# Kernel optimization log

Measured on AMD Instinct MI355X. Metric: run time of the kernel, lower is better.

Reference implementation:

```python
import jax, jax.numpy as jnp
import numpy as np

B, S, D, H = 4, 2048, 768, 12
DH = D // H  # 64


def setup_inputs() -> dict:
    key = jax.random.key(0)
    ks = jax.random.split(key, 7)
    return {
        "sequences": jax.random.normal(ks[0], (B, S, D), dtype=jnp.float32),
        "wq": jax.random.normal(ks[1], (H, DH, DH), dtype=jnp.float32) / np.sqrt(DH),
        "bq": jax.random.normal(ks[2], (H, DH), dtype=jnp.float32) * 0.02,
        "wk": jax.random.normal(ks[3], (H, DH, DH), dtype=jnp.float32) / np.sqrt(DH),
        "bk": jax.random.normal(ks[4], (H, DH), dtype=jnp.float32) * 0.02,
        "wv": jax.random.normal(ks[5], (H, DH, DH), dtype=jnp.float32) / np.sqrt(DH),
        "bv": jax.random.normal(ks[6], (H, DH), dtype=jnp.float32) * 0.02,
    }


def reference(sequences, wq, bq, wk, bk, wv, bv):
    # split channels into heads: [B, S, H, DH]
    xh = sequences.reshape(B, S, H, DH)
    # per-head linear projections (weight applied as x @ W^T + b, matching nn.Linear)
    q = jnp.einsum("bshd,hed->bshe", xh, wq) + bq  # [B,S,H,DH]
    k = jnp.einsum("bshd,hed->bshe", xh, wk) + bk
    v = jnp.einsum("bshd,hed->bshe", xh, wv) + bv
    scale = 1.0 / np.sqrt(DH).astype(np.float32)
    scores = jnp.einsum("bqhd,bkhd->bhqk", q, k) * scale  # [B,H,S,S]
    attn = jax.nn.softmax(scores, axis=-1)
    out = jnp.einsum("bhqk,bkhd->bqhd", attn, v)  # [B,S,H,DH]
    return out.reshape(B, S, D)
```

## Files before the change

kernel.cpp:

```cpp
#include <hip/hip_runtime.h>

#define NB 4
#define NS 2048
#define ND 768
#define NH 12
#define NDH 64
#define XPITCH 72
#define SSCALE 0.18033688011112043f

typedef __bf16 bf16x8 __attribute__((ext_vector_type(8)));
typedef float  f32x4  __attribute__((ext_vector_type(4)));
typedef unsigned int u32;

#define MFMA16(a, b, c) __builtin_amdgcn_mfma_f32_16x16x32_bf16(a, b, c, 0, 0, 0)

__device__ __forceinline__ u32 packbf(float a, float b) {
    u32 ua = __builtin_bit_cast(u32, a) + 0x8000u;
    u32 ub = __builtin_bit_cast(u32, b) + 0x8000u;
    return __builtin_amdgcn_perm(ub, ua, 0x07060302u);
}

__device__ __forceinline__ bf16x8 cvt8(float4 a, float4 b) {
    union { u32 u[4]; bf16x8 v; } r;
    r.u[0] = packbf(a.x, a.y); r.u[1] = packbf(a.z, a.w);
    r.u[2] = packbf(b.x, b.y); r.u[3] = packbf(b.z, b.w);
    return r.v;
}

__device__ __forceinline__ __bf16 f2bf(float f) {
    u32 u = __builtin_bit_cast(u32, f) + 0x8000u;
    unsigned short s = (unsigned short)(u >> 16);
    return __builtin_bit_cast(__bf16, s);
}

__device__ __forceinline__ void gl16(const __bf16* g, __bf16* l) {
    __builtin_amdgcn_global_load_lds(
        (const __attribute__((address_space(1))) unsigned int*)g,
        (__attribute__((address_space(3))) unsigned int*)l,
        16, 0, 0);
}


__global__ __launch_bounds__(256, 4) void proj_kernel(
    const float* __restrict__ x,
    const float* __restrict__ wq, const float* __restrict__ bq,
    const float* __restrict__ wk, const float* __restrict__ bk,
    const float* __restrict__ wv, const float* __restrict__ bv,
    __bf16* __restrict__ qws, __bf16* __restrict__ kws, __bf16* __restrict__ vtws)
{
    const int st = blockIdx.x, h = blockIdx.y, b = blockIdx.z;
    const int s0 = st * 64;
    const int tid = threadIdx.x;

    __shared__ __align__(16) __bf16 Xs[64 * XPITCH];
    __shared__ __align__(16) __bf16 Tv[64 * XPITCH];

    const int r = tid >> 2, f = tid & 3;
    const int lane = tid & 63, w = tid >> 6, col = lane & 15, quad = lane >> 4;

    const size_t wrow = (size_t)(h * NDH + w * 16 + col) * NDH;
    const float* wq0 = wq + wrow + quad * 8;
    const float* wk0 = wk + wrow + quad * 8;
    const float* wv0 = wv + wrow + quad * 8;
    const bf16x8 wqa0 = cvt8(*(const float4*)(wq0),      *(const float4*)(wq0 + 4));
    const bf16x8 wqa1 = cvt8(*(const float4*)(wq0 + 32), *(const float4*)(wq0 + 36));
    const bf16x8 wka0 = cvt8(*(const float4*)(wk0),      *(const float4*)(wk0 + 4));
    const bf16x8 wka1 = cvt8(*(const float4*)(wk0 + 32), *(const float4*)(wk0 + 36));
    const bf16x8 wva0 = cvt8(*(const float4*)(wv0),      *(const float4*)(wv0 + 4));
    const bf16x8 wva1 = cvt8(*(const float4*)(wv0 + 32), *(const float4*)(wv0 + 36));

    float bqs[4], bks[4], bvs[4];
#pragma unroll
    for (int rr = 0; rr < 4; ++rr) {
        const int e = h * NDH + w * 16 + quad * 4 + rr;
        bqs[rr] = bq[e] * SSCALE;
        bks[rr] = bk[e];
        bvs[rr] = bv[e];
    }

    const size_t bh = (size_t)(b * NH + h);

    {
        const float* xrow = x + (size_t)(b * NS + s0 + r) * ND + h * NDH + f * 16;
        const float4 v0 = *(const float4*)(xrow);
        const float4 v1 = *(const float4*)(xrow + 4);
        const float4 v2 = *(const float4*)(xrow + 8);
        const float4 v3 = *(const float4*)(xrow + 12);
        *(bf16x8*)&Xs[r * XPITCH + f * 16]     = cvt8(v0, v1);
        *(bf16x8*)&Xs[r * XPITCH + f * 16 + 8] = cvt8(v2, v3);
    }
    __syncthreads();

    const int e0 = w * 16 + quad * 4;
    const int jj = e0 >> 5;
    const int qa = (e0 >> 3) & 3;
    const int hf = (e0 >> 2) & 1;
    const int Lf = qa * 16 + col;
    const int kt = st >> 1;

#pragma unroll
    for (int nt = 0; nt < 4; ++nt) {
        const bf16x8 xb0 = *(const bf16x8*)&Xs[(nt * 16 + col) * XPITCH + quad * 8];
        const bf16x8 xb1 = *(const bf16x8*)&Xs[(nt * 16 + col) * XPITCH + 32 + quad * 8];
        f32x4 aq = {0.f, 0.f, 0.f, 0.f};
        f32x4 ak = {0.f, 0.f, 0.f, 0.f};
        f32x4 av = {0.f, 0.f, 0.f, 0.f};
        aq = MFMA16(wqa0, xb0, aq); aq = MFMA16(wqa1, xb1, aq);
        ak = MFMA16(wka0, xb0, ak); ak = MFMA16(wka1, xb1, ak);
        av = MFMA16(wva0, xb0, av); av = MFMA16(wva1, xb1, av);

        union { u32 u[2]; uint2 v; } pq, pk;
        pq.u[0] = packbf(fmaf(aq[0], SSCALE, bqs[0]), fmaf(aq[1], SSCALE, bqs[1]));
        pq.u[1] = packbf(fmaf(aq[2], SSCALE, bqs[2]), fmaf(aq[3], SSCALE, bqs[3]));
        pk.u[0] = packbf(ak[0] + bks[0], ak[1] + bks[1]);
        pk.u[1] = packbf(ak[2] + bks[2], ak[3] + bks[3]);

        const int wa = (st & 1) * 2 + (nt >> 1);
        const int mt = nt & 1;
        const size_t kidx = ((((((size_t)bh * 16 + kt) * 4 + wa) * 2 + mt) * 2 + jj) * 64 + Lf) * 8 + hf * 4;
        const size_t qidx = (((((size_t)bh * 32 + st) * 4 + nt) * 2 + jj) * 64 + Lf) * 8 + hf * 4;
        *(uint2*)(kws + kidx) = pk.v;
        *(uint2*)(qws + qidx) = pq.v;

        const int pos = ((nt >> 1) << 5) + ((col >> 2) << 3) + ((nt & 1) << 2) + (col & 3);
#pragma unroll
        for (int rr = 0; rr < 4; ++rr)
            Tv[(w * 16 + quad * 4 + rr) * XPITCH + pos] = f2bf(av[rr] + bvs[rr]);
    }
    __syncthreads();

    {
        const uint4 v0 = *(const uint4*)&Tv[r * XPITCH + f * 16];
        const uint4 v1 = *(const uint4*)&Tv[r * XPITCH + f * 16 + 8];
        const int wv_ = (st & 1) * 2 + (f >> 1);
        const int dtv = r >> 4;
        const int colv = r & 15;
        const int L0 = ((f & 1) * 2 + 0) * 16 + colv;
        const int L1 = ((f & 1) * 2 + 1) * 16 + colv;
        const size_t vbase = (((size_t)bh * 16 + kt) * 4 + wv_) * 4 + dtv;
        *(uint4*)(vtws + (vbase * 64 + L0) * 8) = v0;
        *(uint4*)(vtws + (vbase * 64 + L1) * 8) = v1;
    }
}

__global__ __launch_bounds__(256, 4) void attn_kernel(
    const __bf16* __restrict__ qws, const __bf16* __restrict__ kws,
    const __bf16* __restrict__ vtws, float* __restrict__ out)
{
    const int bid = blockIdx.x;
    const int xcd = bid & 7;
    const int j   = bid >> 3;
    const int g   = xcd * 6 + (j >> 5);
    const int qt  = j & 31;
    const int h   = g % NH;
    const int b   = g / NH;

    const int q0 = qt * 64;
    const int tid = threadIdx.x;

    __shared__ __align__(16) unsigned char smem[33280];
    __bf16* ldsK = (__bf16*)smem;
    float* slab  = (float*)smem;
    float* lbuf  = (float*)(smem + 32768);

    const size_t bh = (size_t)(b * NH + h);
    const int lane = tid & 63, w = tid >> 6, col = lane & 15, quad = lane >> 4;
    const int wq = w >> 1, wk = w & 1;

    bf16x8 qb0[2], qb1[2];
    {
        const __bf16* qp = qws + (size_t)bh * 131072 + (size_t)qt * 4096
                         + wq * 2048 + lane * 8;
#pragma unroll
        for (int nt = 0; nt < 2; ++nt) {
            qb0[nt] = *(const bf16x8*)(qp + nt * 1024);
            qb1[nt] = *(const bf16x8*)(qp + nt * 1024 + 512);
        }
    }

    const __bf16* kg = kws  + (size_t)bh * 131072 + wk * 2048 + lane * 8;
    const __bf16* vg = vtws + (size_t)bh * 131072 + wk * 2048 + lane * 8;
    __bf16* lk0 = ldsK + w * 2048;
    __bf16* lk1 = ldsK + 8192 + w * 2048;
    const __bf16* lkr0 = lk0 + lane * 8;
    const __bf16* lkr1 = lk1 + lane * 8;

    float l[2] = {0.f, 0.f};
    f32x4 o[4][2];
#pragma unroll
    for (int dt = 0; dt < 4; ++dt)
#pragma unroll
        for (int nt = 0; nt < 2; ++nt) o[dt][nt] = (f32x4){0.f, 0.f, 0.f, 0.f};

#define ATTN_ITER(ktv, LKRD, LKN, DMA_C, PV_LAST) do {                        \
        const __bf16* _vp = vg + (size_t)(ktv) * 4096;                        \
        const bf16x8 va0 = *(const bf16x8*)(_vp);                             \
        const bf16x8 va1 = *(const bf16x8*)(_vp + 512);                       \
        const bf16x8 va2 = *(const bf16x8*)(_vp + 1024);                      \
        const bf16x8 va3 = *(const bf16x8*)(_vp + 1536);                      \
        __builtin_amdgcn_sched_barrier(0);                                    \
        asm volatile("s_waitcnt vmcnt(4)" ::: "memory");                      \
        __builtin_amdgcn_sched_barrier(0);                                    \
        const bf16x8 ka00 = *(const bf16x8*)(LKRD);                           \
        const bf16x8 ka01 = *(const bf16x8*)(LKRD + 512);                     \
        const bf16x8 ka10 = *(const bf16x8*)(LKRD + 1024);                    \
        const bf16x8 ka11 = *(const bf16x8*)(LKRD + 1536);                    \
        if (DMA_C) {                                                          \
            const __bf16* _kn = kg + (size_t)((ktv) + 1) * 4096;              \
            gl16(_kn,        LKN);        gl16(_kn + 512,  LKN + 512);        \
            gl16(_kn + 1024, LKN + 1024); gl16(_kn + 1536, LKN + 1536);       \
        }                                                                     \
        union { u32 u[4]; bf16x8 v; } pb[2];                                  \
        _Pragma("unroll")                                                     \
        for (int nt = 0; nt < 2; ++nt) {                                      \
            f32x4 sA = {0.f, 0.f, 0.f, 0.f};                                  \
            f32x4 sB = {0.f, 0.f, 0.f, 0.f};                                  \
            sA = MFMA16(ka00, qb0[nt], sA); sA = MFMA16(ka01, qb1[nt], sA);   \
            sB = MFMA16(ka10, qb0[nt], sB); sB = MFMA16(ka11, qb1[nt], sB);   \
            const float p0 = __builtin_amdgcn_exp2f(sA[0]);                   \
            const float p1 = __builtin_amdgcn_exp2f(sA[1]);                   \
            const float p2 = __builtin_amdgcn_exp2f(sA[2]);                   \
            const float p3 = __builtin_amdgcn_exp2f(sA[3]);                   \
            const float p4 = __builtin_amdgcn_exp2f(sB[0]);                   \
            const float p5 = __builtin_amdgcn_exp2f(sB[1]);                   \
            const float p6 = __builtin_amdgcn_exp2f(sB[2]);                   \
            const float p7 = __builtin_amdgcn_exp2f(sB[3]);                   \
            l[nt] += ((p0 + p1) + (p2 + p3)) + ((p4 + p5) + (p6 + p7));       \
            pb[nt].u[0] = packbf(p0, p1);                                     \
            pb[nt].u[1] = packbf(p2, p3);                                     \
            pb[nt].u[2] = packbf(p4, p5);                                     \
            pb[nt].u[3] = packbf(p6, p7);                                     \
        }                                                                     \
        __builtin_amdgcn_sched_barrier(0);                                    \
        if (PV_LAST) { asm volatile("s_waitcnt vmcnt(0)" ::: "memory"); }     \
        else         { asm volatile("s_waitcnt vmcnt(4)" ::: "memory"); }     \
        __builtin_amdgcn_sched_barrier(0);                                    \
        _Pragma("unroll")                                                     \
        for (int nt = 0; nt < 2; ++nt) {                                      \
            o[0][nt] = MFMA16(va0, pb[nt].v, o[0][nt]);                       \
            o[1][nt] = MFMA16(va1, pb[nt].v, o[1][nt]);                       \
            o[2][nt] = MFMA16(va2, pb[nt].v, o[2][nt]);                       \
            o[3][nt] = MFMA16(va3, pb[nt].v, o[3][nt]);                       \
        }                                                                     \
    } while (0)

    gl16(kg,        lk0);        gl16(kg + 512,  lk0 + 512);
    gl16(kg + 1024, lk0 + 1024); gl16(kg + 1536, lk0 + 1536);

    for (int kt2 = 0; kt2 < 30; kt2 += 2) {
        ATTN_ITER(kt2,     lkr0, lk1, true, false);
        ATTN_ITER(kt2 + 1, lkr1, lk0, true, false);
    }
    ATTN_ITER(30, lkr0, lk1, true,  false);
    ATTN_ITER(31, lkr1, lk0, false, true);
#undef ATTN_ITER

#pragma unroll
    for (int nt = 0; nt < 2; ++nt) {
        l[nt] += __shfl_xor(l[nt], 16, 64);
        l[nt] += __shfl_xor(l[nt], 32, 64);
    }

    __syncthreads();
    if (quad == 0) {
#pragma unroll
        for (int nt = 0; nt < 2; ++nt)
            lbuf[wk * 64 + wq * 32 + nt * 16 + col] = l[nt];
    }
    __syncthreads();

    float scale[2];
#pragma unroll
    for (int nt = 0; nt < 2; ++nt) {
        const int ri = wq * 32 + nt * 16 + col;
        scale[nt] = 1.0f / (lbuf[ri] + lbuf[64 + ri]);
    }
#pragma unroll
    for (int dt = 0; dt < 4; ++dt)
#pragma unroll
        for (int nt = 0; nt < 2; ++nt) o[dt][nt] *= scale[nt];

    if (wk == 0) {
#pragma unroll
        for (int dt = 0; dt < 4; ++dt)
#pragma unroll
            for (int nt = 0; nt < 2; ++nt)
                *(f32x4*)&slab[(wq * 32 + nt * 16 + col) * 68 + dt * 16 + quad * 4] = o[dt][nt];
    }
    __syncthreads();
    if (wk == 1) {
#pragma unroll
        for (int dt = 0; dt < 4; ++dt)
#pragma unroll
            for (int nt = 0; nt < 2; ++nt) {
                f32x4* p = (f32x4*)&slab[(wq * 32 + nt * 16 + col) * 68 + dt * 16 + quad * 4];
                *p = *p + o[dt][nt];
            }
    }
    __syncthreads();

    const int qr = tid >> 2, fq = tid & 3;
#pragma unroll
    for (int j2 = 0; j2 < 4; ++j2) {
        const f32x4 a = *(const f32x4*)&slab[qr * 68 + fq * 16 + j2 * 4];
        *(f32x4*)&out[(size_t)(b * NS + q0 + qr) * ND + h * NDH + fq * 16 + j2 * 4] = a;
    }
}

extern "C" void kernel_launch(void* const* d_in, const int* in_sizes, int n_in,
                              void* d_out, int out_size, void* d_ws, size_t ws_size,
                              hipStream_t stream) {
    (void)in_sizes; (void)n_in; (void)out_size; (void)ws_size;
    const float* x  = (const float*)d_in[0];
    const float* wq = (const float*)d_in[1];
    const float* bq = (const float*)d_in[2];
    const float* wk = (const float*)d_in[3];
    const float* bk = (const float*)d_in[4];
    const float* wv = (const float*)d_in[5];
    const float* bv = (const float*)d_in[6];
    float* out = (float*)d_out;

    __bf16* qws  = (__bf16*)d_ws;
    __bf16* kws  = qws + (size_t)NB * NH * NS * NDH;
    __bf16* vtws = kws + (size_t)NB * NH * NS * NDH;

    dim3 grid(NS / 64, NH, NB);
    proj_kernel<<<grid, 256, 0, stream>>>(x, wq, bq, wk, bk, wv, bv, qws, kws, vtws);
    attn_kernel<<<dim3(NS / 64 * NH * NB), 256, 0, stream>>>(qws, kws, vtws, out);
}
```

Measured before the change: 162.5 us.

## Process two query tiles per attention block to reuse K/V loads

Each attention workgroup now handles two 64-row query tiles instead of one, so every K tile staged in LDS and every V fragment loaded from global memory feeds twice as many MFMA operations. The grid is halved to 768 blocks, the XCD-aware block-to-head mapping is adjusted to match, and launch bounds drop to 3 waves per SIMD to make room for the doubled Q fragments and accumulators. The epilogue is looped over the two tiles with extra barriers. The cost is higher register pressure and lower occupancy, and fewer blocks may leave part of the GPU underused.

```diff
diff --git a/kernel.cpp b/kernel.cpp
--- a/kernel.cpp
+++ b/kernel.cpp
@@ -143,19 +143,18 @@
     }
 }
 
-__global__ __launch_bounds__(256, 4) void attn_kernel(
+__global__ __launch_bounds__(256, 3) void attn_kernel(
     const __bf16* __restrict__ qws, const __bf16* __restrict__ kws,
     const __bf16* __restrict__ vtws, float* __restrict__ out)
 {
     const int bid = blockIdx.x;
     const int xcd = bid & 7;
     const int j   = bid >> 3;
-    const int g   = xcd * 6 + (j >> 5);
-    const int qt  = j & 31;
+    const int g   = xcd * 6 + (j >> 4);
+    const int qtp = j & 15;
     const int h   = g % NH;
     const int b   = g / NH;
 
-    const int q0 = qt * 64;
     const int tid = threadIdx.x;
 
     __shared__ __align__(16) unsigned char smem[33280];
@@ -167,15 +166,17 @@
     const int lane = tid & 63, w = tid >> 6, col = lane & 15, quad = lane >> 4;
     const int wq = w >> 1, wk = w & 1;
 
-    bf16x8 qb0[2], qb1[2];
+    bf16x8 qb0[2][2], qb1[2][2];
     {
-        const __bf16* qp = qws + (size_t)bh * 131072 + (size_t)qt * 4096
+        const __bf16* qp = qws + (size_t)bh * 131072 + (size_t)qtp * 8192
                          + wq * 2048 + lane * 8;
 #pragma unroll
-        for (int nt = 0; nt < 2; ++nt) {
-            qb0[nt] = *(const bf16x8*)(qp + nt * 1024);
-            qb1[nt] = *(const bf16x8*)(qp + nt * 1024 + 512);
-        }
+        for (int q2 = 0; q2 < 2; ++q2)
+#pragma unroll
+            for (int nt = 0; nt < 2; ++nt) {
+                qb0[q2][nt] = *(const bf16x8*)(qp + q2 * 4096 + nt * 1024);
+                qb1[q2][nt] = *(const bf16x8*)(qp + q2 * 4096 + nt * 1024 + 512);
+            }
     }
 
     const __bf16* kg = kws  + (size_t)bh * 131072 + wk * 2048 + lane * 8;
@@ -185,12 +186,53 @@
     const __bf16* lkr0 = lk0 + lane * 8;
     const __bf16* lkr1 = lk1 + lane * 8;
 
-    float l[2] = {0.f, 0.f};
-    f32x4 o[4][2];
-#pragma unroll
-    for (int dt = 0; dt < 4; ++dt)
-#pragma unroll
-        for (int nt = 0; nt < 2; ++nt) o[dt][nt] = (f32x4){0.f, 0.f, 0.f, 0.f};
+    float l[2][2] = {{0.f, 0.f}, {0.f, 0.f}};
+    f32x4 o[2][4][2];
+#pragma unroll
+    for (int q2 = 0; q2 < 2; ++q2)
+#pragma unroll
+        for (int dt = 0; dt < 4; ++dt)
+#pragma unroll
+            for (int nt = 0; nt < 2; ++nt) o[q2][dt][nt] = (f32x4){0.f, 0.f, 0.f, 0.f};
+
+#define QKPV(q2, DO_WAIT, PV_LAST) do {                                       \
+        union { u32 u[4]; bf16x8 v; } pb[2];                                  \
+        _Pragma("unroll")                                                     \
+        for (int nt = 0; nt < 2; ++nt) {                                      \
+            f32x4 sA = {0.f, 0.f, 0.f, 0.f};                                  \
+            f32x4 sB = {0.f, 0.f, 0.f, 0.f};                                  \
+            sA = MFMA16(ka00, qb0[q2][nt], sA);                               \
+            sA = MFMA16(ka01, qb1[q2][nt], sA);                               \
+            sB = MFMA16(ka10, qb0[q2][nt], sB);                               \
+            sB = MFMA16(ka11, qb1[q2][nt], sB);                               \
+            const float p0 = __builtin_amdgcn_exp2f(sA[0]);                   \
+            const float p1 = __builtin_amdgcn_exp2f(sA[1]);                   \
+            const float p2 = __builtin_amdgcn_exp2f(sA[2]);                   \
+            const float p3 = __builtin_amdgcn_exp2f(sA[3]);                   \
+            const float p4 = __builtin_amdgcn_exp2f(sB[0]);                   \
+            const float p5 = __builtin_amdgcn_exp2f(sB[1]);                   \
+            const float p6 = __builtin_amdgcn_exp2f(sB[2]);                   \
+            const float p7 = __builtin_amdgcn_exp2f(sB[3]);                   \
+            l[q2][nt] += ((p0 + p1) + (p2 + p3)) + ((p4 + p5) + (p6 + p7));   \
+            pb[nt].u[0] = packbf(p0, p1);                                     \
+            pb[nt].u[1] = packbf(p2, p3);                                     \
+            pb[nt].u[2] = packbf(p4, p5);                                     \
+            pb[nt].u[3] = packbf(p6, p7);                                     \
+        }                                                                     \
+        if (DO_WAIT) {                                                        \
+            __builtin_amdgcn_sched_barrier(0);                                \
+            if (PV_LAST) { asm volatile("s_waitcnt vmcnt(0)" ::: "memory"); } \
+            else         { asm volatile("s_waitcnt vmcnt(4)" ::: "memory"); } \
+            __builtin_amdgcn_sched_barrier(0);                                \
+        }                                                                     \
+        _Pragma("unroll")                                                     \
+        for (int nt = 0; nt < 2; ++nt) {                                      \
+            o[q2][0][nt] = MFMA16(va0, pb[nt].v, o[q2][0][nt]);               \
+            o[q2][1][nt] = MFMA16(va1, pb[nt].v, o[q2][1][nt]);               \
+            o[q2][2][nt] = MFMA16(va2, pb[nt].v, o[q2][2][nt]);               \
+            o[q2][3][nt] = MFMA16(va3, pb[nt].v, o[q2][3][nt]);               \
+        }                                                                     \
+    } while (0)
 
 #define ATTN_ITER(ktv, LKRD, LKN, DMA_C, PV_LAST) do {                        \
         const __bf16* _vp = vg + (size_t)(ktv) * 4096;                        \
@@ -210,38 +252,8 @@
             gl16(_kn,        LKN);        gl16(_kn + 512,  LKN + 512);        \
             gl16(_kn + 1024, LKN + 1024); gl16(_kn + 1536, LKN + 1536);       \
         }                                                                     \
-        union { u32 u[4]; bf16x8 v; } pb[2];                                  \
-        _Pragma("unroll")                                                     \
-        for (int nt = 0; nt < 2; ++nt) {                                      \
-            f32x4 sA = {0.f, 0.f, 0.f, 0.f};                                  \
-            f32x4 sB = {0.f, 0.f, 0.f, 0.f};                                  \
-            sA = MFMA16(ka00, qb0[nt], sA); sA = MFMA16(ka01, qb1[nt], sA);   \
-            sB = MFMA16(ka10, qb0[nt], sB); sB = MFMA16(ka11, qb1[nt], sB);   \
-            const float p0 = __builtin_amdgcn_exp2f(sA[0]);                   \
-            const float p1 = __builtin_amdgcn_exp2f(sA[1]);                   \
-            const float p2 = __builtin_amdgcn_exp2f(sA[2]);                   \
-            const float p3 = __builtin_amdgcn_exp2f(sA[3]);                   \
-            const float p4 = __builtin_amdgcn_exp2f(sB[0]);                   \
-            const float p5 = __builtin_amdgcn_exp2f(sB[1]);                   \
-            const float p6 = __builtin_amdgcn_exp2f(sB[2]);                   \
-            const float p7 = __builtin_amdgcn_exp2f(sB[3]);                   \
-            l[nt] += ((p0 + p1) + (p2 + p3)) + ((p4 + p5) + (p6 + p7));       \
-            pb[nt].u[0] = packbf(p0, p1);                                     \
-            pb[nt].u[1] = packbf(p2, p3);                                     \
-            pb[nt].u[2] = packbf(p4, p5);                                     \
-            pb[nt].u[3] = packbf(p6, p7);                                     \
-        }                                                                     \
-        __builtin_amdgcn_sched_barrier(0);                                    \
-        if (PV_LAST) { asm volatile("s_waitcnt vmcnt(0)" ::: "memory"); }     \
-        else         { asm volatile("s_waitcnt vmcnt(4)" ::: "memory"); }     \
-        __builtin_amdgcn_sched_barrier(0);                                    \
-        _Pragma("unroll")                                                     \
-        for (int nt = 0; nt < 2; ++nt) {                                      \
-            o[0][nt] = MFMA16(va0, pb[nt].v, o[0][nt]);                       \
-            o[1][nt] = MFMA16(va1, pb[nt].v, o[1][nt]);                       \
-            o[2][nt] = MFMA16(va2, pb[nt].v, o[2][nt]);                       \
-            o[3][nt] = MFMA16(va3, pb[nt].v, o[3][nt]);                       \
-        }                                                                     \
+        { QKPV(0, true, PV_LAST); }                                           \
+        { QKPV(1, false, false); }                                            \
     } while (0)
 
     gl16(kg,        lk0);        gl16(kg + 512,  lk0 + 512);
@@ -254,56 +266,66 @@
     ATTN_ITER(30, lkr0, lk1, true,  false);
     ATTN_ITER(31, lkr1, lk0, false, true);
 #undef ATTN_ITER
-
-#pragma unroll
-    for (int nt = 0; nt < 2; ++nt) {
-        l[nt] += __shfl_xor(l[nt], 16, 64);
-        l[nt] += __shfl_xor(l[nt], 32, 64);
-    }
+#undef QKPV
+
+#pragma unroll
+    for (int q2 = 0; q2 < 2; ++q2)
+#pragma unroll
+        for (int nt = 0; nt < 2; ++nt) {
+            l[q2][nt] += __shfl_xor(l[q2][nt], 16, 64);
+            l[q2][nt] += __shfl_xor(l[q2][nt], 32, 64);
+        }
 
     __syncthreads();
-    if (quad == 0) {
-#pragma unroll
-        for (int nt = 0; nt < 2; ++nt)
-            lbuf[wk * 64 + wq * 32 + nt * 16 + col] = l[nt];
-    }
-    __syncthreads();
-
-    float scale[2];
-#pragma unroll
-    for (int nt = 0; nt < 2; ++nt) {
-        const int ri = wq * 32 + nt * 16 + col;
-        scale[nt] = 1.0f / (lbuf[ri] + lbuf[64 + ri]);
-    }
-#pragma unroll
-    for (int dt = 0; dt < 4; ++dt)
-#pragma unroll
-        for (int nt = 0; nt < 2; ++nt) o[dt][nt] *= scale[nt];
-
-    if (wk == 0) {
+
+#pragma unroll
+    for (int q2 = 0; q2 < 2; ++q2) {
+        const int q0 = (qtp * 2 + q2) * 64;
+
+        if (quad == 0) {
+#pragma unroll
+            for (int nt = 0; nt < 2; ++nt)
+                lbuf[wk * 64 + wq * 32 + nt * 16 + col] = l[q2][nt];
+        }
+        __syncthreads();
+
+        float scale[2];
+#pragma unroll
+        for (int nt = 0; nt < 2; ++nt) {
+            const int ri = wq * 32 + nt * 16 + col;
+            scale[nt] = 1.0f / (lbuf[ri] + lbuf[64 + ri]);
+        }
 #pragma unroll
         for (int dt = 0; dt < 4; ++dt)
 #pragma unroll
-            for (int nt = 0; nt < 2; ++nt)
-                *(f32x4*)&slab[(wq * 32 + nt * 16 + col) * 68 + dt * 16 + quad * 4] = o[dt][nt];
-    }
-    __syncthreads();
-    if (wk == 1) {
-#pragma unroll
-        for (int dt = 0; dt < 4; ++dt)
-#pragma unroll
-            for (int nt = 0; nt < 2; ++nt) {
-                f32x4* p = (f32x4*)&slab[(wq * 32 + nt * 16 + col) * 68 + dt * 16 + quad * 4];
-                *p = *p + o[dt][nt];
-            }
-    }
-    __syncthreads();
-
-    const int qr = tid >> 2, fq = tid & 3;
-#pragma unroll
-    for (int j2 = 0; j2 < 4; ++j2) {
-        const f32x4 a = *(const f32x4*)&slab[qr * 68 + fq * 16 + j2 * 4];
-        *(f32x4*)&out[(size_t)(b * NS + q0 + qr) * ND + h * NDH + fq * 16 + j2 * 4] = a;
+            for (int nt = 0; nt < 2; ++nt) o[q2][dt][nt] *= scale[nt];
+
+        if (wk == 0) {
+#pragma unroll
+            for (int dt = 0; dt < 4; ++dt)
+#pragma unroll
+                for (int nt = 0; nt < 2; ++nt)
+                    *(f32x4*)&slab[(wq * 32 + nt * 16 + col) * 68 + dt * 16 + quad * 4] = o[q2][dt][nt];
+        }
+        __syncthreads();
+        if (wk == 1) {
+#pragma unroll
+            for (int dt = 0; dt < 4; ++dt)
+#pragma unroll
+                for (int nt = 0; nt < 2; ++nt) {
+                    f32x4* p = (f32x4*)&slab[(wq * 32 + nt * 16 + col) * 68 + dt * 16 + quad * 4];
+                    *p = *p + o[q2][dt][nt];
+                }
+        }
+        __syncthreads();
+
+        const int qr = tid >> 2, fq = tid & 3;
+#pragma unroll
+        for (int j2 = 0; j2 < 4; ++j2) {
+            const f32x4 a = *(const f32x4*)&slab[qr * 68 + fq * 16 + j2 * 4];
+            *(f32x4*)&out[(size_t)(b * NS + q0 + qr) * ND + h * NDH + fq * 16 + j2 * 4] = a;
+        }
+        __syncthreads();
     }
 }
 
@@ -326,5 +348,5 @@
 
     dim3 grid(NS / 64, NH, NB);
     proj_kernel<<<grid, 256, 0, stream>>>(x, wq, bq, wk, bk, wv, bv, qws, kws, vtws);
-    attn_kernel<<<dim3(NS / 64 * NH * NB), 256, 0, stream>>>(qws, kws, vtws, out);
-}
+    attn_kernel<<<dim3(768), 256, 0, stream>>>(qws, kws, vtws, out);
+}
```

Measured after the change: 300.1 us. 84.6% more time.
